# Optimization experiments

Hardware: AMD Instinct MI355X
Metric: run time of the kernel (lower is better)

The kernel has to match this reference:

```python
import jax, jax.numpy as jnp
import numpy as np
import math

TAU = 2.0
EPS = 1e-5
ALPHA = 2.0  # spikingjelly surrogate.ATan default alpha

@jax.custom_vjp
def atan_spike(x):
    return (x >= 0.0).astype(x.dtype)

def _spike_fwd(x):
    return atan_spike(x), x

def _spike_bwd(x, g):
    s = math.pi / 2.0 * ALPHA
    return (g * (ALPHA / 2.0) / (1.0 + (s * x) ** 2),)

atan_spike.defvjp(_spike_fwd, _spike_bwd)

def lif_seq(x_seq):
    # MultiStepLIFNode: v' = v + (x - v)/tau ; spike = H(v'-1) ; hard reset to v_reset=0
    def step(v, x):
        v = v + (x - v) / TAU
        s = atan_spike(v - 1.0)
        v = v * (1.0 - jax.lax.stop_gradient(s))  # detach_reset=True
        return v, s
    _, s_seq = jax.lax.scan(step, jnp.zeros_like(x_seq[0]), x_seq)
    return s_seq

def setup_inputs() -> dict:
    key = jax.random.key(0)
    kx, kw = jax.random.split(key)
    T, B, N, P, D = 4, 64, 1024, 63, 128
    x = jax.random.normal(kx, (T, B, N, P), dtype=jnp.float32)
    W = jax.random.normal(kw, (D, P), dtype=jnp.float32) * np.float32(1.0 / np.sqrt(P))
    gamma = jnp.ones((D,), dtype=jnp.float32)
    beta = jnp.zeros((D,), dtype=jnp.float32)
    return {"x": x, "W": W, "gamma": gamma, "beta": beta, "pe": 0}

def reference(x, W, gamma, beta, pe):
    # bias-free Linear: [T,B,N,P] x [D,P] -> [T,B,N,D]
    h = jnp.einsum('tbnp,dp->tbnd', x, W)
    # BatchNorm1d over channel D; training-mode batch stats over (T*B, N)
    mean = jnp.mean(h, axis=(0, 1, 2), keepdims=True)
    var = jnp.var(h, axis=(0, 1, 2), keepdims=True)  # biased, as torch BN normalization
    h = (h - mean) * jax.lax.rsqrt(var + EPS) * gamma + beta
    # multi-step LIF across T (self.pe=False -> tAPE branch skipped)
    out = lif_seq(h)  # [T,B,N,D] == original output after final transpose
    return out
```

## Files before the change

kernel.cpp:

```cpp
#include <hip/hip_runtime.h>
#include <math.h>

#define T_STEPS 4
#define R_ROWS  65536
#define M_ROWS  262144
#define P_DIM   63
#define D_DIM   128
#define PP      64

#define TILES_TOTAL (M_ROWS / 64)
#define G_CHUNKS 8

typedef float v4f __attribute__((ext_vector_type(4)));

__global__ __launch_bounds__(256) void gram_kernel(const float* __restrict__ x,
                                                   double* __restrict__ partials,
                                                   int tiles_per_block) {
    __shared__ __align__(16) float xt[2][64 * PP];
    const int tid = threadIdx.x;
    const int tj = tid & 15;
    const int ti = tid >> 4;

    double dacc[4][4];
#pragma unroll
    for (int a = 0; a < 4; a++)
#pragma unroll
        for (int b = 0; b < 4; b++) dacc[a][b] = 0.0;

    if (tid < 64) {
        xt[0][tid * PP + 63] = 1.0f;
        xt[1][tid * PP + 63] = 1.0f;
    }

    const int tile0 = blockIdx.x * tiles_per_block;
    float4 reg[4];

    {
        const float4* src = (const float4*)(x + (size_t)tile0 * (64 * 63));
#pragma unroll
        for (int it = 0; it < 4; it++) {
            int k = tid + it * 256;
            reg[it] = (k < 1008) ? src[k] : make_float4(0.f, 0.f, 0.f, 0.f);
        }
    }
#pragma unroll
    for (int it = 0; it < 4; it++) {
        int k = tid + it * 256;
        if (k < 1008) {
            const float* ve = (const float*)&reg[it];
            int flat = k * 4;
#pragma unroll
            for (int e = 0; e < 4; e++) {
                int f = flat + e;
                int r = f / 63;
                int c = f - r * 63;
                xt[0][r * PP + c] = ve[e];
            }
        }
    }
    __syncthreads();

    for (int t = 0; t < tiles_per_block; t++) {
        const int cur = t & 1;
        if (t + 1 < tiles_per_block) {
            const float4* src = (const float4*)(x + (size_t)(tile0 + t + 1) * (64 * 63));
#pragma unroll
            for (int it = 0; it < 4; it++) {
                int k = tid + it * 256;
                reg[it] = (k < 1008) ? src[k] : make_float4(0.f, 0.f, 0.f, 0.f);
            }
        }

        float facc[4][4];
#pragma unroll
        for (int a = 0; a < 4; a++)
#pragma unroll
            for (int b = 0; b < 4; b++) facc[a][b] = 0.0f;

        const float* buf = xt[cur];
        for (int r = 0; r < 64; r++) {
            float4 xi = *(const float4*)&buf[r * PP + ti * 4];
            float4 xj = *(const float4*)&buf[r * PP + tj * 4];
            const float* xia = (const float*)&xi;
            const float* xja = (const float*)&xj;
#pragma unroll
            for (int a = 0; a < 4; a++)
#pragma unroll
                for (int b = 0; b < 4; b++)
                    facc[a][b] = fmaf(xia[a], xja[b], facc[a][b]);
        }
#pragma unroll
        for (int a = 0; a < 4; a++)
#pragma unroll
            for (int b = 0; b < 4; b++) dacc[a][b] += (double)facc[a][b];

        __syncthreads();
        if (t + 1 < tiles_per_block) {
            float* nbuf = xt[1 - cur];
#pragma unroll
            for (int it = 0; it < 4; it++) {
                int k = tid + it * 256;
                if (k < 1008) {
                    const float* ve = (const float*)&reg[it];
                    int flat = k * 4;
#pragma unroll
                    for (int e = 0; e < 4; e++) {
                        int f = flat + e;
                        int r = f / 63;
                        int c = f - r * 63;
                        nbuf[r * PP + c] = ve[e];
                    }
                }
            }
            __syncthreads();
        }
    }

    double* Pb = partials + (size_t)blockIdx.x * 4096;
#pragma unroll
    for (int a = 0; a < 4; a++)
#pragma unroll
        for (int b = 0; b < 4; b++)
            Pb[(ti * 4 + a) * 64 + (tj * 4 + b)] = dacc[a][b];
}

__global__ __launch_bounds__(256) void reduce_kernel(const double* __restrict__ partials,
                                                     double* __restrict__ G8,
                                                     int copies_per_chunk) {
    const int chunk = blockIdx.x >> 4;
    const int idx   = (blockIdx.x & 15) * 256 + threadIdx.x;
    const double* src = partials + (size_t)chunk * copies_per_chunk * 4096;
    double s = 0.0;
    for (int c = 0; c < copies_per_chunk; c++)
        s += src[(size_t)c * 4096 + idx];
    G8[(size_t)chunk * 4096 + idx] = s;
}

__global__ __launch_bounds__(64) void stats_kernel(const double* __restrict__ G,
                                                   const float* __restrict__ W,
                                                   const float* __restrict__ gamma,
                                                   const float* __restrict__ beta,
                                                   float* __restrict__ stats) {
    const int d = blockIdx.x;
    const int p = threadIdx.x;
    __shared__ float sW[64];
    sW[p] = (p < P_DIM) ? W[d * P_DIM + p] : 0.0f;
    __syncthreads();

    double inner = 0.0;
#pragma unroll
    for (int c = 0; c < G_CHUNKS; c++) {
        const double* Gr = G + (size_t)c * (64 * 64) + p * 64;
        for (int q = 0; q < 64; q++) inner += Gr[q] * (double)sW[q];
    }

    double contrib = (double)sW[p] * inner;
    double ex2M = contrib;
#pragma unroll
    for (int off = 32; off > 0; off >>= 1) ex2M += __shfl_down(ex2M, off, 64);
    double meanM = __shfl(inner, 63, 64);

    if (p == 0) {
        double mean = meanM / (double)M_ROWS;
        double ex2  = ex2M  / (double)M_ROWS;
        double var  = ex2 - mean * mean;
        float varf  = (float)var;
        float vpe   = varf + 1e-5f;
        float invstd = (float)(1.0 / sqrt((double)vpe));
        stats[d * 4 + 0] = (float)mean;
        stats[d * 4 + 1] = invstd;
        stats[d * 4 + 2] = gamma[d];
        stats[d * 4 + 3] = beta[d];
    }
}

#define LIF_ROWS 16
#define SW_STRIDE 132
#define SX_STRIDE 64
__global__ __launch_bounds__(256) void lif_kernel(const float* __restrict__ x,
                                                  const float* __restrict__ W,
                                                  const float* __restrict__ stats,
                                                  float* __restrict__ out) {
    __shared__ __align__(16) float sw[P_DIM * SW_STRIDE];
    __shared__ __align__(16) float sx[T_STEPS * LIF_ROWS * SX_STRIDE];
    const int tid = threadIdx.x;

    for (int k = tid; k < P_DIM * D_DIM; k += 256) {
        int d = k / 63;
        int p = k - d * 63;
        sw[p * SW_STRIDE + d] = W[k];
    }

    const int r0 = blockIdx.x * LIF_ROWS;
    const int seg = tid >> 6;
    const int lane = tid & 63;
    const v4f* src = (const v4f*)(x + ((size_t)seg * R_ROWS + r0) * P_DIM);
    for (int k = lane; k < 252; k += 64) {
        v4f v = __builtin_nontemporal_load(&src[k]);
        int flat = k * 4;
#pragma unroll
        for (int e = 0; e < 4; e++) {
            int f = flat + e;
            int r = f / 63;
            int c = f - r * 63;
            sx[(seg * LIF_ROWS + r) * SX_STRIDE + c] = v[e];
        }
    }
    __syncthreads();

    const int td = tid & 31;
    const int tr = tid >> 5;
    const int d0 = td * 4;
    const int rowa = tr * 2;

    float acc[8][4];
#pragma unroll
    for (int u = 0; u < 8; u++)
#pragma unroll
        for (int j = 0; j < 4; j++) acc[u][j] = 0.0f;

    for (int pq = 0; pq < 15; pq++) {
        const int p = pq * 4;
        float4 w0 = *(const float4*)&sw[(p + 0) * SW_STRIDE + d0];
        float4 w1 = *(const float4*)&sw[(p + 1) * SW_STRIDE + d0];
        float4 w2 = *(const float4*)&sw[(p + 2) * SW_STRIDE + d0];
        float4 w3 = *(const float4*)&sw[(p + 3) * SW_STRIDE + d0];
#pragma unroll
        for (int t = 0; t < T_STEPS; t++)
#pragma unroll
            for (int i = 0; i < 2; i++) {
                float4 xv = *(const float4*)&sx[(t * LIF_ROWS + rowa + i) * SX_STRIDE + p];
                float* a = acc[t * 2 + i];
                a[0] = fmaf(xv.x, w0.x, a[0]);
                a[1] = fmaf(xv.x, w0.y, a[1]);
                a[2] = fmaf(xv.x, w0.z, a[2]);
                a[3] = fmaf(xv.x, w0.w, a[3]);
                a[0] = fmaf(xv.y, w1.x, a[0]);
                a[1] = fmaf(xv.y, w1.y, a[1]);
                a[2] = fmaf(xv.y, w1.z, a[2]);
                a[3] = fmaf(xv.y, w1.w, a[3]);
                a[0] = fmaf(xv.z, w2.x, a[0]);
                a[1] = fmaf(xv.z, w2.y, a[1]);
                a[2] = fmaf(xv.z, w2.z, a[2]);
                a[3] = fmaf(xv.z, w2.w, a[3]);
                a[0] = fmaf(xv.w, w3.x, a[0]);
                a[1] = fmaf(xv.w, w3.y, a[1]);
                a[2] = fmaf(xv.w, w3.z, a[2]);
                a[3] = fmaf(xv.w, w3.w, a[3]);
            }
    }
#pragma unroll
    for (int p = 60; p < 63; p++) {
        float4 w4 = *(const float4*)&sw[p * SW_STRIDE + d0];
#pragma unroll
        for (int t = 0; t < T_STEPS; t++)
#pragma unroll
            for (int i = 0; i < 2; i++) {
                float xv = sx[(t * LIF_ROWS + rowa + i) * SX_STRIDE + p];
                float* a = acc[t * 2 + i];
                a[0] = fmaf(xv, w4.x, a[0]);
                a[1] = fmaf(xv, w4.y, a[1]);
                a[2] = fmaf(xv, w4.z, a[2]);
                a[3] = fmaf(xv, w4.w, a[3]);
            }
    }

#pragma unroll
    for (int i = 0; i < 2; i++) {
        const int row = r0 + rowa + i;
        float sval[T_STEPS][4];
#pragma unroll
        for (int j = 0; j < 4; j++) {
            float4 st = ((const float4*)stats)[d0 + j];
            float v = 0.0f;
#pragma unroll
            for (int t = 0; t < T_STEPS; t++) {
                float hn = (acc[t * 2 + i][j] - st.x) * st.y;
                hn = hn * st.z;
                hn = hn + st.w;
                v = v + (hn - v) * 0.5f;
                float s = (v >= 1.0f) ? 1.0f : 0.0f;
                sval[t][j] = s;
                if (s != 0.0f) v = 0.0f;
            }
        }
#pragma unroll
        for (int t = 0; t < T_STEPS; t++) {
            v4f o = {sval[t][0], sval[t][1], sval[t][2], sval[t][3]};
            __builtin_nontemporal_store(
                o, (v4f*)&out[((size_t)t * R_ROWS + row) * D_DIM + d0]);
        }
    }
}

extern "C" void kernel_launch(void* const* d_in, const int* in_sizes, int n_in,
                              void* d_out, int out_size, void* d_ws, size_t ws_size,
                              hipStream_t stream) {
    const float* x     = (const float*)d_in[0];
    const float* W     = (const float*)d_in[1];
    const float* gamma = (const float*)d_in[2];
    const float* beta  = (const float*)d_in[3];
    float* out = (float*)d_out;

    const size_t fixed = (size_t)G_CHUNKS * 4096 * 8 + 4096;
    int nparts = 512;
    while (nparts > 64 && (size_t)nparts * 4096 * 8 + fixed > ws_size) nparts >>= 1;
    const int tiles_per_block = TILES_TOTAL / nparts;

    double* partials = (double*)d_ws;
    double* G8       = (double*)((char*)d_ws + (size_t)nparts * 4096 * 8);
    float*  stats    = (float*)((char*)G8 + (size_t)G_CHUNKS * 4096 * 8);

    gram_kernel<<<nparts, 256, 0, stream>>>(x, partials, tiles_per_block);
    reduce_kernel<<<G_CHUNKS * 16, 256, 0, stream>>>(partials, G8, nparts / G_CHUNKS);
    stats_kernel<<<D_DIM, 64, 0, stream>>>(G8, W, gamma, beta, stats);
    lif_kernel<<<R_ROWS / LIF_ROWS, 256, 0, stream>>>(x, W, stats, out);
}
```

Baseline: 292.4 us.

## Use single-wavefront gram blocks with 8x8 register tiles and more blocks

The Gram-matrix kernel now runs one 64-thread wavefront per block, and each thread accumulates an 8x8 sub-tile instead of 4x4. Because there is only one wave, the shared-memory double buffer and all __syncthreads barriers are removed, and the number of partial blocks rises from 512 to 2048. This aims for more FMA reuse per LDS load, no barrier cost and more blocks in flight. In exchange it drops the register prefetch overlap and raises register pressure from 64 double accumulators per thread, and the reduce kernel has more partials to sum.

```diff
diff --git a/kernel.cpp b/kernel.cpp
--- a/kernel.cpp
+++ b/kernel.cpp
@@ -13,115 +13,73 @@
 
 typedef float v4f __attribute__((ext_vector_type(4)));
 
-__global__ __launch_bounds__(256) void gram_kernel(const float* __restrict__ x,
-                                                   double* __restrict__ partials,
-                                                   int tiles_per_block) {
-    __shared__ __align__(16) float xt[2][64 * PP];
+__global__ __launch_bounds__(64) void gram_kernel(const float* __restrict__ x,
+                                                  double* __restrict__ partials,
+                                                  int tiles_per_block) {
+    __shared__ __align__(16) float xt[64 * PP];
     const int tid = threadIdx.x;
-    const int tj = tid & 15;
-    const int ti = tid >> 4;
-
-    double dacc[4][4];
-#pragma unroll
-    for (int a = 0; a < 4; a++)
-#pragma unroll
-        for (int b = 0; b < 4; b++) dacc[a][b] = 0.0;
-
-    if (tid < 64) {
-        xt[0][tid * PP + 63] = 1.0f;
-        xt[1][tid * PP + 63] = 1.0f;
-    }
+    const int ti = tid >> 3;
+    const int tj = tid & 7;
+
+    double dacc[8][8];
+#pragma unroll
+    for (int a = 0; a < 8; a++)
+#pragma unroll
+        for (int b = 0; b < 8; b++) dacc[a][b] = 0.0;
+
+    xt[tid * PP + 63] = 1.0f;
 
     const int tile0 = blockIdx.x * tiles_per_block;
-    float4 reg[4];
-
-    {
-        const float4* src = (const float4*)(x + (size_t)tile0 * (64 * 63));
-#pragma unroll
-        for (int it = 0; it < 4; it++) {
-            int k = tid + it * 256;
-            reg[it] = (k < 1008) ? src[k] : make_float4(0.f, 0.f, 0.f, 0.f);
-        }
-    }
-#pragma unroll
-    for (int it = 0; it < 4; it++) {
-        int k = tid + it * 256;
-        if (k < 1008) {
-            const float* ve = (const float*)&reg[it];
+    for (int t = 0; t < tiles_per_block; t++) {
+        const float4* src = (const float4*)(x + (size_t)(tile0 + t) * (64 * 63));
+        for (int k = tid; k < 1008; k += 64) {
+            float4 v = src[k];
+            const float* ve = (const float*)&v;
             int flat = k * 4;
 #pragma unroll
             for (int e = 0; e < 4; e++) {
                 int f = flat + e;
                 int r = f / 63;
                 int c = f - r * 63;
-                xt[0][r * PP + c] = ve[e];
-            }
-        }
-    }
-    __syncthreads();
-
-    for (int t = 0; t < tiles_per_block; t++) {
-        const int cur = t & 1;
-        if (t + 1 < tiles_per_block) {
-            const float4* src = (const float4*)(x + (size_t)(tile0 + t + 1) * (64 * 63));
-#pragma unroll
-            for (int it = 0; it < 4; it++) {
-                int k = tid + it * 256;
-                reg[it] = (k < 1008) ? src[k] : make_float4(0.f, 0.f, 0.f, 0.f);
-            }
-        }
-
-        float facc[4][4];
-#pragma unroll
-        for (int a = 0; a < 4; a++)
-#pragma unroll
-            for (int b = 0; b < 4; b++) facc[a][b] = 0.0f;
-
-        const float* buf = xt[cur];
+                xt[r * PP + c] = ve[e];
+            }
+        }
+
+        float facc[8][8];
+#pragma unroll
+        for (int a = 0; a < 8; a++)
+#pragma unroll
+            for (int b = 0; b < 8; b++) facc[a][b] = 0.0f;
+
         for (int r = 0; r < 64; r++) {
-            float4 xi = *(const float4*)&buf[r * PP + ti * 4];
-            float4 xj = *(const float4*)&buf[r * PP + tj * 4];
-            const float* xia = (const float*)&xi;
-            const float* xja = (const float*)&xj;
-#pragma unroll
-            for (int a = 0; a < 4; a++)
-#pragma unroll
-                for (int b = 0; b < 4; b++)
+            const float* row = &xt[r * PP];
+            float4 xi0 = *(const float4*)&row[ti * 8];
+            float4 xi1 = *(const float4*)&row[ti * 8 + 4];
+            float4 xj0 = *(const float4*)&row[tj * 8];
+            float4 xj1 = *(const float4*)&row[tj * 8 + 4];
+            const float xia[8] = {xi0.x, xi0.y, xi0.z, xi0.w,
+                                  xi1.x, xi1.y, xi1.z, xi1.w};
+            const float xja[8] = {xj0.x, xj0.y, xj0.z, xj0.w,
+                                  xj1.x, xj1.y, xj1.z, xj1.w};
+#pragma unroll
+            for (int a = 0; a < 8; a++)
+#pragma unroll
+                for (int b = 0; b < 8; b++)
                     facc[a][b] = fmaf(xia[a], xja[b], facc[a][b]);
         }
 #pragma unroll
-        for (int a = 0; a < 4; a++)
-#pragma unroll
-            for (int b = 0; b < 4; b++) dacc[a][b] += (double)facc[a][b];
-
-        __syncthreads();
-        if (t + 1 < tiles_per_block) {
-            float* nbuf = xt[1 - cur];
-#pragma unroll
-            for (int it = 0; it < 4; it++) {
-                int k = tid + it * 256;
-                if (k < 1008) {
-                    const float* ve = (const float*)&reg[it];
-                    int flat = k * 4;
-#pragma unroll
-                    for (int e = 0; e < 4; e++) {
-                        int f = flat + e;
-                        int r = f / 63;
-                        int c = f - r * 63;
-                        nbuf[r * PP + c] = ve[e];
-                    }
-                }
-            }
-            __syncthreads();
-        }
+        for (int a = 0; a < 8; a++)
+#pragma unroll
+            for (int b = 0; b < 8; b++) dacc[a][b] += (double)facc[a][b];
     }
 
     double* Pb = partials + (size_t)blockIdx.x * 4096;
 #pragma unroll
-    for (int a = 0; a < 4; a++)
-#pragma unroll
-        for (int b = 0; b < 4; b++)
-            Pb[(ti * 4 + a) * 64 + (tj * 4 + b)] = dacc[a][b];
+    for (int a = 0; a < 8; a++) {
+        double* dst = &Pb[(ti * 8 + a) * 64 + tj * 8];
+#pragma unroll
+        for (int b = 0; b < 8; b++) dst[b] = dacc[a][b];
+    }
 }
 
 __global__ __launch_bounds__(256) void reduce_kernel(const double* __restrict__ partials,
@@ -303,15 +261,15 @@
     float* out = (float*)d_out;
 
     const size_t fixed = (size_t)G_CHUNKS * 4096 * 8 + 4096;
-    int nparts = 512;
-    while (nparts > 64 && (size_t)nparts * 4096 * 8 + fixed > ws_size) nparts >>= 1;
+    int nparts = 2048;
+    while (nparts > 256 && (size_t)nparts * 4096 * 8 + fixed > ws_size) nparts >>= 1;
     const int tiles_per_block = TILES_TOTAL / nparts;
 
     double* partials = (double*)d_ws;
     double* G8       = (double*)((char*)d_ws + (size_t)nparts * 4096 * 8);
     float*  stats    = (float*)((char*)G8 + (size_t)G_CHUNKS * 4096 * 8);
 
-    gram_kernel<<<nparts, 256, 0, stream>>>(x, partials, tiles_per_block);
+    gram_kernel<<<nparts, 64, 0, stream>>>(x, partials, tiles_per_block);
     reduce_kernel<<<G_CHUNKS * 16, 256, 0, stream>>>(partials, G8, nparts / G_CHUNKS);
     stats_kernel<<<D_DIM, 64, 0, stream>>>(G8, W, gamma, beta, stats);
     lif_kernel<<<R_ROWS / LIF_ROWS, 256, 0, stream>>>(x, W, stats, out);
```

After: 358.8 us. 22.7% more time.
